# Performance work log

Hardware: AMD Instinct MI355X
Metric: run time of the kernel (lower is better)

Reference implementation:

```python
import jax, jax.numpy as jnp
import numpy as np

# Structural hyperparams (mirror init_kwargs)
G, Q, C, D = 2, 8, 1024, 8          # groups, quantizers/group, codebook_size, codebook_dim
DIMS = 1024                          # residual_fsq.dim
DPG = DIMS // G                      # dim per group (project_out output)
B, L = 4, 4096                       # batch, frame length
UP_K, UP_S = 4, 2                    # upsample ConvTranspose1d kernel/stride
HEAD_K, HEAD_OUT = 7, 512            # head Conv1d kernel / out channels


def setup_inputs() -> dict:
    key = jax.random.key(0)
    ks = jax.random.split(key, 8)
    indices = jax.random.randint(ks[0], (B, G * Q, L), 0, C, dtype=jnp.int64)
    codebooks = jax.random.normal(ks[1], (G, Q, C, D), jnp.float32)
    scales = jax.random.uniform(ks[2], (G, Q, D), jnp.float32, 0.5, 2.0)
    W_out = jax.random.normal(ks[3], (G, D, DPG), jnp.float32) * (1.0 / np.sqrt(D))
    b_out = jnp.zeros((G, DPG), jnp.float32)
    W_up = jax.random.normal(ks[4], (DIMS, DIMS, UP_K), jnp.float32) * 0.02   # IOH layout
    b_up = jnp.zeros((DIMS,), jnp.float32)
    W_head = jax.random.normal(ks[5], (HEAD_OUT, DIMS, HEAD_K), jnp.float32) * 0.02  # OIH
    b_head = jnp.zeros((HEAD_OUT,), jnp.float32)
    return dict(indices=indices, codebooks=codebooks, scales=scales,
                W_out=W_out, b_out=b_out, W_up=W_up, b_up=b_up,
                W_head=W_head, b_head=b_head)


def reference(indices, codebooks, scales, W_out, b_out, W_up, b_up, W_head, b_head):
    b, gq, l = indices.shape
    g, q = codebooks.shape[0], codebooks.shape[1]
    # [B, G*Q, L] -> [G, B, L, Q]  (matches view + permute in forward)
    idx = indices.reshape(b, g, q, l).transpose(1, 0, 3, 2)
    mask = idx == -1                              # dropout-padded codes
    idx0 = jnp.where(mask, 0, idx)
    # gather codes per (group, quantizer): codebooks[g, q, idx0[g,b,l,q]] -> [G,B,L,Q,D]
    g_ix = jnp.arange(g)[:, None, None, None]
    q_ix = jnp.arange(q)[None, None, None, :]
    codes = codebooks[g_ix, q_ix, idx0]
    # mask, scale, sum over quantizers (residual sum)
    codes = jnp.where(mask[..., None], 0.0, codes) * scales[:, None, None, :, :]
    summed = codes.sum(axis=3)                    # [G,B,L,D]
    # per-group project_out: Linear(D -> DPG)
    z = jnp.einsum('gbld,gde->gble', summed, W_out) + b_out[:, None, None, :]
    # concat groups along feature dim -> [B, L, DIMS], then NCH for convs
    z_q = z.transpose(1, 2, 0, 3).reshape(b, l, g * z.shape[-1])
    zc = z_q.transpose(0, 2, 1)                   # [B, DIMS, L]
    # upsample: ConvTranspose1d(DIMS->DIMS, k=4, stride=2) -> [B, DIMS, 2L]
    zu = jax.lax.conv_transpose(zc, W_up, strides=(UP_S,), padding='SAME',
                                dimension_numbers=('NCH', 'IOH', 'NCH'))
    zu = zu + b_up[None, :, None]
    # head: Conv1d(DIMS -> HEAD_OUT, k=7, same padding)
    x = jax.lax.conv_general_dilated(zu, W_head, window_strides=(1,), padding='SAME',
                                     dimension_numbers=('NCH', 'OIH', 'NCH'))
    x = x + b_head[None, :, None]
    return x
```

## Files before the change

### kernel.cpp

```cpp
#include <hip/hip_runtime.h>
#include <hip/hip_bf16.h>

typedef __attribute__((ext_vector_type(8))) short bf16x8;
typedef __attribute__((ext_vector_type(4))) float f32x4;

#define GQ 16
#define L_IN 4096
#define T_UP 8192
#define CB 1024
#define ZROWS 4098
#define UROWS 8198

__device__ __forceinline__ void gload16(const void* g, void* l) {
    __builtin_amdgcn_global_load_lds((const __attribute__((address_space(1))) void*)g,
                                     (__attribute__((address_space(3))) void*)l, 16, 0, 0);
}

__global__ __launch_bounds__(256) void zero_pads(__hip_bfloat16* __restrict__ zp,
                                                 __hip_bfloat16* __restrict__ zup) {
    int idx = blockIdx.x * 256 + threadIdx.x;
    if (idx < 8192) {
        int b = idx >> 11, rs = (idx >> 10) & 1, c = idx & 1023;
        size_t row = (size_t)b * ZROWS + (rs ? (ZROWS - 1) : 0);
        zp[row * 1024 + c] = __float2bfloat16(0.f);
    } else if (idx < 8192 + 24576) {
        int rem = idx - 8192;
        int b = rem / 6144, r2 = rem % 6144;
        int r6 = r2 >> 10, c = r2 & 1023;
        size_t row = (size_t)b * UROWS + (r6 < 3 ? r6 : (UROWS - 6 + r6));
        zup[row * 1024 + c] = __float2bfloat16(0.f);
    }
}

__global__ __launch_bounds__(256) void repack_up(const float* __restrict__ Wup,
                                                 __hip_bfloat16* __restrict__ Wr) {
    int idx = blockIdx.x * 256 + threadIdx.x;
    int kk = idx >> 20;
    int co = (idx >> 10) & 1023;
    int ci = idx & 1023;
    Wr[idx] = __float2bfloat16(Wup[((ci << 10) + co) * 4 + kk]);
}

__global__ __launch_bounds__(256) void repack_head(const float* __restrict__ Wh,
                                                   __hip_bfloat16* __restrict__ Wr) {
    int idx = blockIdx.x * 256 + threadIdx.x;
    int kk = idx >> 19;
    int rem = idx & ((1 << 19) - 1);
    int o = rem >> 10;
    int ci = rem & 1023;
    Wr[idx] = __float2bfloat16(Wh[(o * 1024 + ci) * 7 + kk]);
}

__global__ __launch_bounds__(256) void dequant_project(
    const int* __restrict__ indices, const float* __restrict__ codebooks,
    const float* __restrict__ scales, const float* __restrict__ Wout,
    const float* __restrict__ bout, __hip_bfloat16* __restrict__ z)
{
    __shared__ float w_lds[8192];
    __shared__ float b_lds[1024];
    __shared__ float part[128];
    __shared__ float summed[16];
    int tid = threadIdx.x;
    for (int k = tid; k < 8192; k += 256) w_lds[k] = Wout[k];
    for (int k = tid; k < 1024; k += 256) b_lds[k] = bout[k];
    int p0 = blockIdx.x * 16;
    int b  = p0 >> 12;
    int l0 = p0 & 4095;
    __syncthreads();
    for (int i = 0; i < 16; ++i) {
        int l = l0 + i;
        if (tid < 128) {
            int gq = tid >> 3;
            int d  = tid & 7;
            int idx = indices[(b * GQ + gq) * L_IN + l];
            float v = 0.f;
            if (idx >= 0) {
                int ic = (idx < CB) ? idx : 0;
                v = codebooks[(gq * CB + ic) * 8 + d] * scales[gq * 8 + d];
            }
            part[tid] = v;
        }
        __syncthreads();
        if (tid < 16) {
            int g = tid >> 3, d = tid & 7;
            float s = 0.f;
            for (int q = 0; q < 8; ++q) s += part[(g * 8 + q) * 8 + d];
            summed[tid] = s;
        }
        __syncthreads();
        #pragma unroll
        for (int j = 0; j < 4; ++j) {
            int c = tid + j * 256;
            int g = c >> 9;
            float acc = b_lds[c];
            #pragma unroll
            for (int d = 0; d < 8; ++d)
                acc += summed[g * 8 + d] * w_lds[(g * 8 + d) * 512 + (c & 511)];
            z[((size_t)b * ZROWS + l + 1) * 1024 + c] = __float2bfloat16(acc);
        }
        __syncthreads();
    }
}

__global__ __launch_bounds__(256) void conv_up_mfma(
    const __hip_bfloat16* __restrict__ zp, const __hip_bfloat16* __restrict__ Wr,
    const float* __restrict__ bup, __hip_bfloat16* __restrict__ zup)
{
    __shared__ __hip_bfloat16 Asm[144 * 32];
    __shared__ __hip_bfloat16 Bsm[2 * 128 * 32];
    const int tid = threadIdx.x;
    const int lane = tid & 63;
    const int w = tid >> 6;
    const int co0 = blockIdx.x * 128;
    const int m0 = blockIdx.y * 128;
    const int b = blockIdx.z >> 1, P = blockIdx.z & 1;
    const int wm = w >> 1, wn = w & 1;

    const __hip_bfloat16* zbase = zp + ((size_t)b * ZROWS + m0 + P) * 1024;
    const __hip_bfloat16* wbase = Wr + (size_t)P * (1024 * 1024);

    const f32x4 zero4 = {0.f, 0.f, 0.f, 0.f};
    f32x4 acc[4][4];
#pragma unroll
    for (int r = 0; r < 4; ++r)
#pragma unroll
        for (int c = 0; c < 4; ++c) acc[r][c] = zero4;

    const int l15 = lane & 15;
    const int kq = lane >> 4;

    for (int c0 = 0; c0 < 1024; c0 += 32) {
#pragma unroll
        for (int it = 0; it < 3; ++it) {
            int chunk = it * 256 + tid;
            if (chunk < 516) {
                int row = chunk >> 2, cq = chunk & 3;
                int csrc = cq ^ ((row >> 1) & 3);
                gload16(zbase + (size_t)row * 1024 + c0 + csrc * 8,
                        (char*)Asm + ((it * 256 + (w << 6)) << 4));
            }
        }
#pragma unroll
        for (int it = 0; it < 4; ++it) {
            int chunk = it * 256 + tid;
            int tap = chunk >> 9, rem = chunk & 511;
            int co = rem >> 2, cq = rem & 3;
            int csrc = cq ^ ((co >> 1) & 3);
            gload16(wbase + ((size_t)(tap * 2048 + co0 + co)) * 1024 + c0 + csrc * 8,
                    (char*)Bsm + ((it * 256 + (w << 6)) << 4));
        }
        __syncthreads();

        bf16x8 af[2][4], bfr[2][4];
#pragma unroll
        for (int j = 0; j < 2; ++j)
#pragma unroll
            for (int r = 0; r < 4; ++r) {
                int row = (wm << 6) + r * 16 + l15 + j;
                int pq = kq ^ ((row >> 1) & 3);
                af[j][r] = *(const bf16x8*)&Asm[row * 32 + pq * 8];
            }
#pragma unroll
        for (int j = 0; j < 2; ++j)
#pragma unroll
            for (int c = 0; c < 4; ++c) {
                int row = (wn << 6) + c * 16 + l15;
                int pq = kq ^ ((row >> 1) & 3);
                bfr[j][c] = *(const bf16x8*)&Bsm[j * 4096 + row * 32 + pq * 8];
            }
#pragma unroll
        for (int j = 0; j < 2; ++j)
#pragma unroll
            for (int r = 0; r < 4; ++r)
#pragma unroll
                for (int c = 0; c < 4; ++c)
                    acc[r][c] = __builtin_amdgcn_mfma_f32_16x16x32_bf16(
                        af[j][r], bfr[j][c], acc[r][c], 0, 0, 0);
        __syncthreads();
    }

    const int mrow = (wm << 6) + (kq << 2);
    const int cob = co0 + (wn << 6) + l15;
#pragma unroll
    for (int c = 0; c < 4; ++c) {
        float bias = bup[cob + c * 16];
#pragma unroll
        for (int r = 0; r < 4; ++r)
#pragma unroll
            for (int e = 0; e < 4; ++e) {
                int m = m0 + mrow + r * 16 + e;
                zup[((size_t)b * UROWS + 3 + P + 2 * m) * 1024 + cob + c * 16] =
                    __float2bfloat16(acc[r][c][e] + bias);
            }
    }
}

__global__ __launch_bounds__(256) void conv_head_mfma(
    const __hip_bfloat16* __restrict__ zup, const __hip_bfloat16* __restrict__ Wr,
    const float* __restrict__ bh, float* __restrict__ out)
{
    __shared__ __hip_bfloat16 Asm[144 * 32];
    __shared__ __hip_bfloat16 Bsm[7 * 64 * 32];
    const int tid = threadIdx.x;
    const int lane = tid & 63;
    const int w = tid >> 6;
    const int o0 = blockIdx.x * 64;
    const int t0 = blockIdx.y * 128;
    const int b = blockIdx.z;
    const int wm = w >> 1, wn = w & 1;

    const __hip_bfloat16* zbase = zup + ((size_t)b * UROWS + t0) * 1024;

    const f32x4 zero4 = {0.f, 0.f, 0.f, 0.f};
    f32x4 acc[2][4];
#pragma unroll
    for (int c = 0; c < 2; ++c)
#pragma unroll
        for (int r = 0; r < 4; ++r) acc[c][r] = zero4;

    const int l15 = lane & 15;
    const int kq = lane >> 4;

    for (int c0 = 0; c0 < 1024; c0 += 32) {
#pragma unroll
        for (int it = 0; it < 3; ++it) {
            int chunk = it * 256 + tid;
            if (chunk < 536) {
                int row = chunk >> 2, cq = chunk & 3;
                int csrc = cq ^ ((row >> 1) & 3);
                gload16(zbase + (size_t)row * 1024 + c0 + csrc * 8,
                        (char*)Asm + ((it * 256 + (w << 6)) << 4));
            }
        }
#pragma unroll
        for (int it = 0; it < 7; ++it) {
            int chunk = it * 256 + tid;
            int kk = chunk >> 8, rem = chunk & 255;
            int o = rem >> 2, cq = rem & 3;
            int csrc = cq ^ ((o >> 1) & 3);
            gload16(Wr + ((size_t)(kk * 512 + o0 + o)) * 1024 + c0 + csrc * 8,
                    (char*)Bsm + ((it * 256 + (w << 6)) << 4));
        }
        __syncthreads();

#pragma unroll
        for (int kk = 0; kk < 7; ++kk) {
            bf16x8 wf[2], zf[4];
#pragma unroll
            for (int c = 0; c < 2; ++c) {
                int orow = (wn << 5) + c * 16 + l15;
                int pq = kq ^ ((orow >> 1) & 3);
                wf[c] = *(const bf16x8*)&Bsm[(kk * 64 + orow) * 32 + pq * 8];
            }
#pragma unroll
            for (int r = 0; r < 4; ++r) {
                int row = (wm << 6) + r * 16 + l15 + kk;
                int pq = kq ^ ((row >> 1) & 3);
                zf[r] = *(const bf16x8*)&Asm[row * 32 + pq * 8];
            }
#pragma unroll
            for (int c = 0; c < 2; ++c)
#pragma unroll
                for (int r = 0; r < 4; ++r)
                    acc[c][r] = __builtin_amdgcn_mfma_f32_16x16x32_bf16(
                        wf[c], zf[r], acc[c][r], 0, 0, 0);
        }
        __syncthreads();
    }

    const int ob = o0 + (wn << 5) + (kq << 2);
    const int tb = t0 + (wm << 6) + l15;
#pragma unroll
    for (int c = 0; c < 2; ++c)
#pragma unroll
        for (int e = 0; e < 4; ++e) {
            int o = ob + c * 16 + e;
            float bias = bh[o];
#pragma unroll
            for (int r = 0; r < 4; ++r)
                out[((size_t)b * 512 + o) * T_UP + tb + r * 16] = acc[c][r][e] + bias;
        }
}

extern "C" void kernel_launch(void* const* d_in, const int* in_sizes, int n_in,
                              void* d_out, int out_size, void* d_ws, size_t ws_size,
                              hipStream_t stream) {
    const int*   indices   = (const int*)d_in[0];
    const float* codebooks = (const float*)d_in[1];
    const float* scales    = (const float*)d_in[2];
    const float* Wout      = (const float*)d_in[3];
    const float* bout      = (const float*)d_in[4];
    const float* Wup       = (const float*)d_in[5];
    const float* bup       = (const float*)d_in[6];
    const float* Wh        = (const float*)d_in[7];
    const float* bh        = (const float*)d_in[8];
    float* out = (float*)d_out;

    __hip_bfloat16* zp    = (__hip_bfloat16*)d_ws;
    __hip_bfloat16* zup   = zp + (size_t)4 * ZROWS * 1024;
    __hip_bfloat16* wr_up = zup + (size_t)4 * UROWS * 1024;
    __hip_bfloat16* wr_h  = wr_up + (size_t)4 * 1024 * 1024;

    zero_pads  <<<dim3(128),   dim3(256), 0, stream>>>(zp, zup);
    repack_up  <<<dim3(16384), dim3(256), 0, stream>>>(Wup, wr_up);
    repack_head<<<dim3(14336), dim3(256), 0, stream>>>(Wh, wr_h);
    dequant_project<<<dim3(1024), dim3(256), 0, stream>>>(indices, codebooks, scales,
                                                          Wout, bout, zp);
    conv_up_mfma  <<<dim3(8, 32, 8), dim3(256), 0, stream>>>(zp, wr_up, bup, zup);
    conv_head_mfma<<<dim3(8, 64, 4), dim3(256), 0, stream>>>(zup, wr_h, bh, out);
}
```

Baseline: 516.0 us.

## Double-buffer LDS in both conv GEMMs with 64-wide K steps and larger head tiles

Both MFMA conv kernels now prefetch the next K-slice into a second LDS buffer while computing on the current one, and use 64-channel K steps with an 8-way XOR swizzle. The head conv is restructured to iterate over (tap, channel-chunk) stages with 128x128 tiles instead of 64 outputs by 128 times, so each block loads its weights and shifted activations per tap. Grid order is swapped so the time dimension varies fastest, s_setprio is raised around the MFMA bursts, and launch bounds request two blocks per CU. The larger LDS footprint (64KB per block) and bigger accumulators may limit occupancy, and the head kernel now reloads activation rows per tap instead of reusing one halo tile across all seven taps.

```diff
diff --git a/kernel.cpp b/kernel.cpp
--- a/kernel.cpp
+++ b/kernel.cpp
@@ -102,183 +102,189 @@
     }
 }
 
-__global__ __launch_bounds__(256) void conv_up_mfma(
+__global__ __launch_bounds__(256, 2) void conv_up_mfma(
     const __hip_bfloat16* __restrict__ zp, const __hip_bfloat16* __restrict__ Wr,
     const float* __restrict__ bup, __hip_bfloat16* __restrict__ zup)
 {
-    __shared__ __hip_bfloat16 Asm[144 * 32];
-    __shared__ __hip_bfloat16 Bsm[2 * 128 * 32];
+    __shared__ __hip_bfloat16 Als[2][128][64];
+    __shared__ __hip_bfloat16 Bls[2][128][64];
     const int tid = threadIdx.x;
     const int lane = tid & 63;
     const int w = tid >> 6;
-    const int co0 = blockIdx.x * 128;
-    const int m0 = blockIdx.y * 128;
+    const int wm = w >> 1, wn = w & 1;
+    const int l15 = lane & 15, kq = lane >> 4;
+    const int m0  = blockIdx.x * 128;
+    const int co0 = blockIdx.y * 128;
     const int b = blockIdx.z >> 1, P = blockIdx.z & 1;
-    const int wm = w >> 1, wn = w & 1;
-
-    const __hip_bfloat16* zbase = zp + ((size_t)b * ZROWS + m0 + P) * 1024;
-    const __hip_bfloat16* wbase = Wr + (size_t)P * (1024 * 1024);
+
+    const __hip_bfloat16* zb = zp + ((size_t)b * ZROWS + m0 + P) * 1024;
+    const __hip_bfloat16* wb = Wr + ((size_t)P * 1024 + co0) * 1024;
+
+    auto stage = [&](int buf, int s) {
+        int j = s & 1, ci0 = (s >> 1) << 6;
+        const __hip_bfloat16* sa = zb + (size_t)j * 1024 + ci0;
+        const __hip_bfloat16* sb = wb + (size_t)j * 2048 * 1024 + ci0;
+        #pragma unroll
+        for (int it = 0; it < 4; ++it) {
+            int chunk = it * 256 + tid;
+            int row = chunk >> 3, cs = chunk & 7;
+            int cq = cs ^ (row & 7);
+            gload16(sa + (size_t)row * 1024 + cq * 8,
+                    (char*)&Als[buf][0][0] + ((it * 256 + (w << 6)) << 4));
+            gload16(sb + (size_t)row * 1024 + cq * 8,
+                    (char*)&Bls[buf][0][0] + ((it * 256 + (w << 6)) << 4));
+        }
+    };
 
     const f32x4 zero4 = {0.f, 0.f, 0.f, 0.f};
     f32x4 acc[4][4];
-#pragma unroll
+    #pragma unroll
     for (int r = 0; r < 4; ++r)
-#pragma unroll
+        #pragma unroll
         for (int c = 0; c < 4; ++c) acc[r][c] = zero4;
 
-    const int l15 = lane & 15;
-    const int kq = lane >> 4;
-
-    for (int c0 = 0; c0 < 1024; c0 += 32) {
-#pragma unroll
-        for (int it = 0; it < 3; ++it) {
-            int chunk = it * 256 + tid;
-            if (chunk < 516) {
-                int row = chunk >> 2, cq = chunk & 3;
-                int csrc = cq ^ ((row >> 1) & 3);
-                gload16(zbase + (size_t)row * 1024 + c0 + csrc * 8,
-                        (char*)Asm + ((it * 256 + (w << 6)) << 4));
-            }
-        }
-#pragma unroll
-        for (int it = 0; it < 4; ++it) {
-            int chunk = it * 256 + tid;
-            int tap = chunk >> 9, rem = chunk & 511;
-            int co = rem >> 2, cq = rem & 3;
-            int csrc = cq ^ ((co >> 1) & 3);
-            gload16(wbase + ((size_t)(tap * 2048 + co0 + co)) * 1024 + c0 + csrc * 8,
-                    (char*)Bsm + ((it * 256 + (w << 6)) << 4));
-        }
-        __syncthreads();
-
+    stage(0, 0);
+    __syncthreads();
+    int cur = 0;
+    for (int s = 0; s < 32; ++s) {
+        if (s + 1 < 32) stage(cur ^ 1, s + 1);
         bf16x8 af[2][4], bfr[2][4];
-#pragma unroll
-        for (int j = 0; j < 2; ++j)
-#pragma unroll
+        #pragma unroll
+        for (int sl = 0; sl < 2; ++sl) {
+            #pragma unroll
             for (int r = 0; r < 4; ++r) {
-                int row = (wm << 6) + r * 16 + l15 + j;
-                int pq = kq ^ ((row >> 1) & 3);
-                af[j][r] = *(const bf16x8*)&Asm[row * 32 + pq * 8];
-            }
-#pragma unroll
-        for (int j = 0; j < 2; ++j)
-#pragma unroll
+                int row = (wm << 6) + r * 16 + l15;
+                int pc = (sl * 4 + kq) ^ (row & 7);
+                af[sl][r] = *(const bf16x8*)&Als[cur][row][pc * 8];
+            }
+            #pragma unroll
             for (int c = 0; c < 4; ++c) {
                 int row = (wn << 6) + c * 16 + l15;
-                int pq = kq ^ ((row >> 1) & 3);
-                bfr[j][c] = *(const bf16x8*)&Bsm[j * 4096 + row * 32 + pq * 8];
-            }
-#pragma unroll
-        for (int j = 0; j < 2; ++j)
-#pragma unroll
+                int pc = (sl * 4 + kq) ^ (row & 7);
+                bfr[sl][c] = *(const bf16x8*)&Bls[cur][row][pc * 8];
+            }
+        }
+        __builtin_amdgcn_s_setprio(1);
+        #pragma unroll
+        for (int sl = 0; sl < 2; ++sl)
+            #pragma unroll
             for (int r = 0; r < 4; ++r)
-#pragma unroll
+                #pragma unroll
                 for (int c = 0; c < 4; ++c)
                     acc[r][c] = __builtin_amdgcn_mfma_f32_16x16x32_bf16(
-                        af[j][r], bfr[j][c], acc[r][c], 0, 0, 0);
-        __syncthreads();
-    }
-
-    const int mrow = (wm << 6) + (kq << 2);
+                        af[sl][r], bfr[sl][c], acc[r][c], 0, 0, 0);
+        __builtin_amdgcn_s_setprio(0);
+        __syncthreads();
+        cur ^= 1;
+    }
+
+    const int mb  = m0 + (wm << 6) + (kq << 2);
     const int cob = co0 + (wn << 6) + l15;
-#pragma unroll
+    #pragma unroll
     for (int c = 0; c < 4; ++c) {
         float bias = bup[cob + c * 16];
-#pragma unroll
+        #pragma unroll
         for (int r = 0; r < 4; ++r)
-#pragma unroll
+            #pragma unroll
             for (int e = 0; e < 4; ++e) {
-                int m = m0 + mrow + r * 16 + e;
+                int m = mb + r * 16 + e;
                 zup[((size_t)b * UROWS + 3 + P + 2 * m) * 1024 + cob + c * 16] =
                     __float2bfloat16(acc[r][c][e] + bias);
             }
     }
 }
 
-__global__ __launch_bounds__(256) void conv_head_mfma(
+__global__ __launch_bounds__(256, 2) void conv_head_mfma(
     const __hip_bfloat16* __restrict__ zup, const __hip_bfloat16* __restrict__ Wr,
     const float* __restrict__ bh, float* __restrict__ out)
 {
-    __shared__ __hip_bfloat16 Asm[144 * 32];
-    __shared__ __hip_bfloat16 Bsm[7 * 64 * 32];
+    __shared__ __hip_bfloat16 Als[2][128][64];
+    __shared__ __hip_bfloat16 Bls[2][128][64];
     const int tid = threadIdx.x;
     const int lane = tid & 63;
     const int w = tid >> 6;
-    const int o0 = blockIdx.x * 64;
-    const int t0 = blockIdx.y * 128;
-    const int b = blockIdx.z;
     const int wm = w >> 1, wn = w & 1;
-
-    const __hip_bfloat16* zbase = zup + ((size_t)b * UROWS + t0) * 1024;
+    const int l15 = lane & 15, kq = lane >> 4;
+    const int t0 = blockIdx.x * 128;
+    const int o0 = blockIdx.y * 128;
+    const int b  = blockIdx.z;
+
+    const __hip_bfloat16* wb = Wr + (size_t)o0 * 1024;
+    const __hip_bfloat16* zb = zup + ((size_t)b * UROWS + t0) * 1024;
+
+    auto stage = [&](int buf, int kk, int ci0) {
+        const __hip_bfloat16* sa = wb + (size_t)kk * 512 * 1024 + ci0;
+        const __hip_bfloat16* sb = zb + (size_t)kk * 1024 + ci0;
+        #pragma unroll
+        for (int it = 0; it < 4; ++it) {
+            int chunk = it * 256 + tid;
+            int row = chunk >> 3, cs = chunk & 7;
+            int cq = cs ^ (row & 7);
+            gload16(sa + (size_t)row * 1024 + cq * 8,
+                    (char*)&Als[buf][0][0] + ((it * 256 + (w << 6)) << 4));
+            gload16(sb + (size_t)row * 1024 + cq * 8,
+                    (char*)&Bls[buf][0][0] + ((it * 256 + (w << 6)) << 4));
+        }
+    };
 
     const f32x4 zero4 = {0.f, 0.f, 0.f, 0.f};
-    f32x4 acc[2][4];
-#pragma unroll
-    for (int c = 0; c < 2; ++c)
-#pragma unroll
-        for (int r = 0; r < 4; ++r) acc[c][r] = zero4;
-
-    const int l15 = lane & 15;
-    const int kq = lane >> 4;
-
-    for (int c0 = 0; c0 < 1024; c0 += 32) {
-#pragma unroll
-        for (int it = 0; it < 3; ++it) {
-            int chunk = it * 256 + tid;
-            if (chunk < 536) {
-                int row = chunk >> 2, cq = chunk & 3;
-                int csrc = cq ^ ((row >> 1) & 3);
-                gload16(zbase + (size_t)row * 1024 + c0 + csrc * 8,
-                        (char*)Asm + ((it * 256 + (w << 6)) << 4));
-            }
-        }
-#pragma unroll
-        for (int it = 0; it < 7; ++it) {
-            int chunk = it * 256 + tid;
-            int kk = chunk >> 8, rem = chunk & 255;
-            int o = rem >> 2, cq = rem & 3;
-            int csrc = cq ^ ((o >> 1) & 3);
-            gload16(Wr + ((size_t)(kk * 512 + o0 + o)) * 1024 + c0 + csrc * 8,
-                    (char*)Bsm + ((it * 256 + (w << 6)) << 4));
-        }
-        __syncthreads();
-
-#pragma unroll
-        for (int kk = 0; kk < 7; ++kk) {
-            bf16x8 wf[2], zf[4];
-#pragma unroll
-            for (int c = 0; c < 2; ++c) {
-                int orow = (wn << 5) + c * 16 + l15;
-                int pq = kq ^ ((orow >> 1) & 3);
-                wf[c] = *(const bf16x8*)&Bsm[(kk * 64 + orow) * 32 + pq * 8];
-            }
-#pragma unroll
+    f32x4 acc[4][4];
+    #pragma unroll
+    for (int r = 0; r < 4; ++r)
+        #pragma unroll
+        for (int c = 0; c < 4; ++c) acc[r][c] = zero4;
+
+    int nk = 0, nc = 0;
+    stage(0, nk, nc);
+    if (++nk == 7) { nk = 0; nc += 64; }
+    __syncthreads();
+    int cur = 0;
+    for (int s = 0; s < 112; ++s) {
+        if (s + 1 < 112) {
+            stage(cur ^ 1, nk, nc);
+            if (++nk == 7) { nk = 0; nc += 64; }
+        }
+        bf16x8 af[2][4], bfr[2][4];
+        #pragma unroll
+        for (int sl = 0; sl < 2; ++sl) {
+            #pragma unroll
             for (int r = 0; r < 4; ++r) {
-                int row = (wm << 6) + r * 16 + l15 + kk;
-                int pq = kq ^ ((row >> 1) & 3);
-                zf[r] = *(const bf16x8*)&Asm[row * 32 + pq * 8];
-            }
-#pragma unroll
-            for (int c = 0; c < 2; ++c)
-#pragma unroll
-                for (int r = 0; r < 4; ++r)
-                    acc[c][r] = __builtin_amdgcn_mfma_f32_16x16x32_bf16(
-                        wf[c], zf[r], acc[c][r], 0, 0, 0);
-        }
-        __syncthreads();
-    }
-
-    const int ob = o0 + (wn << 5) + (kq << 2);
-    const int tb = t0 + (wm << 6) + l15;
-#pragma unroll
-    for (int c = 0; c < 2; ++c)
-#pragma unroll
+                int row = (wm << 6) + r * 16 + l15;
+                int pc = (sl * 4 + kq) ^ (row & 7);
+                af[sl][r] = *(const bf16x8*)&Als[cur][row][pc * 8];
+            }
+            #pragma unroll
+            for (int c = 0; c < 4; ++c) {
+                int row = (wn << 6) + c * 16 + l15;
+                int pc = (sl * 4 + kq) ^ (row & 7);
+                bfr[sl][c] = *(const bf16x8*)&Bls[cur][row][pc * 8];
+            }
+        }
+        __builtin_amdgcn_s_setprio(1);
+        #pragma unroll
+        for (int sl = 0; sl < 2; ++sl)
+            #pragma unroll
+            for (int r = 0; r < 4; ++r)
+                #pragma unroll
+                for (int c = 0; c < 4; ++c)
+                    acc[r][c] = __builtin_amdgcn_mfma_f32_16x16x32_bf16(
+                        af[sl][r], bfr[sl][c], acc[r][c], 0, 0, 0);
+        __builtin_amdgcn_s_setprio(0);
+        __syncthreads();
+        cur ^= 1;
+    }
+
+    const int ob = o0 + (wm << 6) + (kq << 2);
+    const int tb = t0 + (wn << 6) + l15;
+    #pragma unroll
+    for (int r = 0; r < 4; ++r)
+        #pragma unroll
         for (int e = 0; e < 4; ++e) {
-            int o = ob + c * 16 + e;
+            int o = ob + r * 16 + e;
             float bias = bh[o];
-#pragma unroll
-            for (int r = 0; r < 4; ++r)
-                out[((size_t)b * 512 + o) * T_UP + tb + r * 16] = acc[c][r][e] + bias;
+            #pragma unroll
+            for (int c = 0; c < 4; ++c)
+                out[((size_t)b * 512 + o) * T_UP + tb + c * 16] = acc[r][c][e] + bias;
         }
 }
 
@@ -306,6 +312,6 @@
     repack_head<<<dim3(14336), dim3(256), 0, stream>>>(Wh, wr_h);
     dequant_project<<<dim3(1024), dim3(256), 0, stream>>>(indices, codebooks, scales,
                                                           Wout, bout, zp);
-    conv_up_mfma  <<<dim3(8, 32, 8), dim3(256), 0, stream>>>(zp, wr_up, bup, zup);
-    conv_head_mfma<<<dim3(8, 64, 4), dim3(256), 0, stream>>>(zup, wr_h, bh, out);
-}
+    conv_up_mfma  <<<dim3(32, 8, 8), dim3(256), 0, stream>>>(zp, wr_up, bup, zup);
+    conv_head_mfma<<<dim3(64, 4, 4), dim3(256), 0, stream>>>(zup, wr_h, bh, out);
+}
```

Result: no change. 514.0 us (-0.4%).
